# Kernel tuning notes

Hardware: AMD Instinct MI355X
Metric: run time of the kernel (lower is better)

## Reference

```python
import jax, jax.numpy as jnp
import numpy as np

R = 2        # pixel-shuffle upscale
CN = 32      # channel_nums
COL = 3      # colors
NM = 6       # module_nums (2 convs each -> 12 backbone convs)
QMAX_A = 255.0   # uint8 activation fake-quant range
QMAX_W = 127.0   # int8 (narrow) weight fake-quant range


def fq_act(x, s):
    # Brevitas Uint8ActPerTensorFloat fake-quant with STE
    v = x / s
    q = jnp.clip(jnp.round(v), 0.0, QMAX_A)
    return s * (v + jax.lax.stop_gradient(q - v))


def fq_w(w, s):
    # Int8WeightPerTensorFloat (symmetric, narrow range) fake-quant with STE
    v = w / s
    q = jnp.clip(jnp.round(v), -QMAX_W, QMAX_W)
    return s * (v + jax.lax.stop_gradient(q - v))


def conv3(x, w, b):
    y = jax.lax.conv_general_dilated(
        x, w, window_strides=(1, 1), padding=((1, 1), (1, 1)),
        dimension_numbers=("NCHW", "OIHW", "NCHW"))
    return y + b[None, :, None, None]


def qblock(x, w, b, sw, act_s):
    # QuantConv3X3: quant_in -> quant conv (+bias) -> QuantReLU (relu + quant)
    xq = fq_act(x, act_s)
    y = conv3(xq, fq_w(w, sw), b)
    y = jax.nn.relu(y)
    return fq_act(y, act_s)


def pixel_shuffle(x, r):
    B, C, H, W = x.shape
    c = C // (r * r)
    x = x.reshape(B, c, r, r, H, W)
    x = x.transpose(0, 1, 4, 2, 5, 3)   # B, c, H, r, W, r
    return x.reshape(B, c, H * r, W * r)


def _forward(x, head_w, head_b, head_sw, bb_w, bb_b, bb_sw, tr_w, tr_b, tr_sw, act_s):
    y0 = qblock(x, head_w, head_b, head_sw, act_s)

    def step(y, p):
        w, b, sw = p
        return qblock(y, w, b, sw, act_s), None

    y, _ = jax.lax.scan(step, y0, (bb_w, bb_b, bb_sw))
    y = qblock(y + y0, tr_w, tr_b, tr_sw, act_s)   # act_type='linear' still hits QuantReLU branch
    y = jnp.clip(y, 0.0, 255.0)
    return pixel_shuffle(y, R)


def setup_inputs() -> dict:
    key = jax.random.key(0)
    ks = jax.random.split(key, 4)
    B, H, W = 8, 256, 256
    x = jax.random.uniform(ks[0], (B, COL, H, W), dtype=jnp.float32) * 255.0
    head_w = jax.random.normal(ks[1], (CN, COL, 3, 3), dtype=jnp.float32) * 0.05
    head_b = jnp.zeros((CN,), jnp.float32)
    bb_w = jax.random.normal(ks[2], (2 * NM, CN, CN, 3, 3), dtype=jnp.float32) * 0.05
    bb_b = jnp.zeros((2 * NM, CN), jnp.float32)
    tr_w = jax.random.normal(ks[3], (COL * R * R, CN, 3, 3), dtype=jnp.float32) * 0.05
    tr_b = jnp.zeros((COL * R * R,), jnp.float32)
    head_sw = jnp.max(jnp.abs(head_w)) / QMAX_W
    bb_sw = jnp.max(jnp.abs(bb_w), axis=(1, 2, 3, 4)) / QMAX_W
    tr_sw = jnp.max(jnp.abs(tr_w)) / QMAX_W
    act_s = jnp.float32(1.0)
    return dict(x=x, head_w=head_w, head_b=head_b, head_sw=head_sw,
                bb_w=bb_w, bb_b=bb_b, bb_sw=bb_sw,
                tr_w=tr_w, tr_b=tr_b, tr_sw=tr_sw, act_s=act_s)


def reference(x, head_w, head_b, head_sw, bb_w, bb_b, bb_sw, tr_w, tr_b, tr_sw, act_s):
    return _forward(x, head_w, head_b, head_sw, bb_w, bb_b, bb_sw, tr_w, tr_b, tr_sw, act_s)
```

## Files before the change

### kernel.cpp

```cpp
#include <hip/hip_runtime.h>

typedef __bf16 bf16x8 __attribute__((ext_vector_type(8)));
typedef float  f32x16 __attribute__((ext_vector_type(16)));

__global__ __launch_bounds__(256) void quantw_kernel(
    const float* __restrict__ src, float* __restrict__ dst,
    const float* __restrict__ sw, int per_layer_sw, int OC, int ICK, int total)
{
    int i = blockIdx.x * 256 + threadIdx.x;
    if (i >= total) return;
    int per = OC * ICK;
    int l = i / per;
    int rem = i - l * per;
    int oc = rem / ICK;
    int k = rem - oc * ICK;
    float s = sw[per_layer_sw ? l : 0];
    float v = rintf(src[i] / s);
    v = fminf(fmaxf(v, -127.0f), 127.0f);
    dst[l * per + k * OC + oc] = v;
}

__global__ __launch_bounds__(256) void packb_kernel(
    const float* __restrict__ src, unsigned short* __restrict__ dst,
    const float* __restrict__ sw, int per_layer_sw, int OC_real, int total)
{
    int i = blockIdx.x * 256 + threadIdx.x;
    if (i >= total) return;
    int l   = i / 9216;
    int r   = i - l * 9216;
    int s   = r >> 9;
    int lane = (r >> 3) & 63;
    int j   = r & 7;
    int k   = s * 16 + ((lane >> 5) << 3) + j;
    int tap = k >> 5;
    int ic  = k & 31;
    int oc  = lane & 31;
    unsigned short v = 0;
    if (oc < OC_real) {
        float scale = sw[per_layer_sw ? l : 0];
        float w = src[((l * OC_real + oc) * 32 + ic) * 9 + tap];
        float q = rintf(w / scale);
        q = fminf(fmaxf(q, -127.0f), 127.0f);
        union { float f; unsigned int u; } cv; cv.f = q;
        v = (unsigned short)(cv.u >> 16);
    }
    dst[i] = v;
}

__global__ __launch_bounds__(256) void head_kernel(
    const float* __restrict__ x, const float* __restrict__ wq,
    const float* __restrict__ bias, const float* __restrict__ sw_ptr,
    const float* __restrict__ s_ptr, unsigned char* __restrict__ out)
{
    __shared__ unsigned char tile[3][10][34];
    const int tid = threadIdx.x;
    const int x0 = blockIdx.x * 32;
    const int y0 = blockIdx.y * 8;
    const int b  = blockIdx.z;
    const float s = s_ptr[0];

    for (int ch = 0; ch < 3; ++ch) {
        const int base = (b * 3 + ch) << 16;
        for (int p = tid; p < 10 * 34; p += 256) {
            int r = p / 34, c = p - r * 34;
            int gy = y0 + r - 1, gx = x0 + c - 1;
            unsigned char v = 0;
            if ((unsigned)gy < 256u && (unsigned)gx < 256u) {
                float xv = x[base + (gy << 8) + gx];
                float q = (s == 1.0f) ? xv : (xv / s);
                q = rintf(q);
                q = fminf(fmaxf(q, 0.0f), 255.0f);
                v = (unsigned char)q;
            }
            tile[ch][r][c] = v;
        }
    }
    __syncthreads();

    const int c = tid & 31, r = tid >> 5;
    float acc[32];
    #pragma unroll
    for (int i = 0; i < 32; ++i) acc[i] = 0.0f;

    #pragma unroll
    for (int ic = 0; ic < 3; ++ic) {
        float a[9];
        #pragma unroll
        for (int dy = 0; dy < 3; ++dy)
            #pragma unroll
            for (int dx = 0; dx < 3; ++dx)
                a[dy * 3 + dx] = (float)tile[ic][r + dy][c + dx];
        #pragma unroll
        for (int t = 0; t < 9; ++t) {
            const float* wrow = wq + (ic * 9 + t) * 32;
            #pragma unroll
            for (int oc = 0; oc < 32; ++oc)
                acc[oc] = fmaf(a[t], wrow[oc], acc[oc]);
        }
    }

    const float alpha = s * sw_ptr[0];
    unsigned int w8[8] = {0,0,0,0,0,0,0,0};
    #pragma unroll
    for (int oc = 0; oc < 32; ++oc) {
        float y = fmaf(alpha, acc[oc], bias[oc]);
        y = fmaxf(y, 0.0f);
        float v = (s == 1.0f) ? y : (y / s);
        v = rintf(v);
        v = fminf(fmaxf(v, 0.0f), 255.0f);
        w8[oc >> 2] |= ((unsigned int)(unsigned char)v) << (8 * (oc & 3));
    }
    uint4* dst = (uint4*)(out + (size_t)((((b << 8) + (y0 + r)) << 8) + (x0 + c)) * 32);
    dst[0] = make_uint4(w8[0], w8[1], w8[2], w8[3]);
    dst[1] = make_uint4(w8[4], w8[5], w8[6], w8[7]);
}

template<bool FINAL>
__global__ __launch_bounds__(256, 4) void qconv_mfma_kernel(
    const unsigned char* __restrict__ in,
    const unsigned char* __restrict__ resid,
    const unsigned short* __restrict__ Bp,
    const float* __restrict__ bias,
    const float* __restrict__ sw_ptr, int sw_idx,
    const float* __restrict__ s_ptr,
    void* __restrict__ out)
{
    __shared__ uint4 aT[2448];
    const int tid = threadIdx.x;
    const int x0 = blockIdx.x << 5;
    const int y0 = blockIdx.y << 4;
    const int b  = blockIdx.z;

    #pragma unroll
    for (int it = 0; it < 5; ++it) {
        int ci = tid + it * 256;
        if (ci < 1224) {
            int yt  = ci / 68;
            int rem = ci - yt * 68;
            int xt  = rem >> 1;
            int ch  = rem & 1;
            int gy = y0 + yt - 1;
            int gx = x0 + xt - 1;
            uint4 raw = make_uint4(0, 0, 0, 0);
            uint4 res = make_uint4(0, 0, 0, 0);
            if ((unsigned)gy < 256u && (unsigned)gx < 256u) {
                size_t off = (size_t)((((b << 8) + gy) << 8) + gx) * 32 + (ch << 4);
                raw = *(const uint4*)(in + off);
                if (FINAL) res = *(const uint4*)(resid + off);
            }
            unsigned int ow[8];
            const unsigned int* rw = (const unsigned int*)&raw;
            const unsigned int* rr = (const unsigned int*)&res;
            #pragma unroll
            for (int w = 0; w < 4; ++w) {
                unsigned int v = rw[w], rv = rr[w];
                #pragma unroll
                for (int hb = 0; hb < 2; ++hb) {
                    unsigned int a0 = (v >> (16 * hb)) & 0xffu;
                    unsigned int a1 = (v >> (16 * hb + 8)) & 0xffu;
                    if (FINAL) {
                        a0 += (rv >> (16 * hb)) & 0xffu;      if (a0 > 255u) a0 = 255u;
                        a1 += (rv >> (16 * hb + 8)) & 0xffu;  if (a1 > 255u) a1 = 255u;
                    }
                    union { float f; unsigned int u; } c0, c1;
                    c0.f = (float)a0; c1.f = (float)a1;
                    ow[2 * w + hb] = (c0.u >> 16) | (c1.u & 0xffff0000u);
                }
            }
            int swz  = (xt & 3) ^ ((xt >> 2) & 3);
            int base = (yt * 34 + xt) << 2;
            aT[base + (((ch << 1) + 0) ^ swz)] = make_uint4(ow[0], ow[1], ow[2], ow[3]);
            aT[base + (((ch << 1) + 1) ^ swz)] = make_uint4(ow[4], ow[5], ow[6], ow[7]);
        }
    }
    __syncthreads();

    const int lane = tid & 63;
    const int wid  = tid >> 6;
    const int px   = lane & 31;
    const int half = lane >> 5;
    const int py0  = wid << 2;

    const bf16x8* Wg = (const bf16x8*)Bp;

    f32x16 acc[4];
    #pragma unroll
    for (int p = 0; p < 4; ++p)
        #pragma unroll
        for (int i = 0; i < 16; ++i) acc[p][i] = 0.0f;

    #pragma unroll
    for (int ich = 0; ich < 2; ++ich) {
        const int cb = (ich << 1) + half;
        #pragma unroll
        for (int dx = 0; dx < 3; ++dx) {
            const int xt = px + dx;
            const int cbs = cb ^ ((xt & 3) ^ ((xt >> 2) & 3));
            bf16x8 af[6];
            #pragma unroll
            for (int yl = 0; yl < 6; ++yl)
                af[yl] = *(const bf16x8*)&aT[((py0 + yl) * 34 + xt) * 4 + cbs];
            #pragma unroll
            for (int dy = 0; dy < 3; ++dy) {
                bf16x8 wfr = Wg[(((dy * 3 + dx) << 1) + ich) * 64 + lane];
                acc[0] = __builtin_amdgcn_mfma_f32_32x32x16_bf16(wfr, af[dy + 0], acc[0], 0, 0, 0);
                acc[1] = __builtin_amdgcn_mfma_f32_32x32x16_bf16(wfr, af[dy + 1], acc[1], 0, 0, 0);
                acc[2] = __builtin_amdgcn_mfma_f32_32x32x16_bf16(wfr, af[dy + 2], acc[2], 0, 0, 0);
                acc[3] = __builtin_amdgcn_mfma_f32_32x32x16_bf16(wfr, af[dy + 3], acc[3], 0, 0, 0);
            }
        }
    }

    const float s = s_ptr[0];
    const float alpha = s * sw_ptr[sw_idx];
    const int gx = x0 + px;

    if (!FINAL) {
        float bv[16];
        #pragma unroll
        for (int r = 0; r < 16; ++r)
            bv[r] = bias[(r & 3) + ((r >> 2) << 3) + (half << 2)];
        #pragma unroll
        for (int py = 0; py < 4; ++py) {
            const int gy = y0 + py0 + py;
            unsigned char* pout = (unsigned char*)out + (((size_t)((((b << 8) + gy) << 8) + gx)) << 5);
            #pragma unroll
            for (int q = 0; q < 4; ++q) {
                unsigned int wv = 0;
                #pragma unroll
                for (int j = 0; j < 4; ++j) {
                    float y = fmaf(alpha, acc[py][4 * q + j], bv[4 * q + j]);
                    y = fmaxf(y, 0.0f);
                    float v = (s == 1.0f) ? y : (y / s);
                    v = rintf(v);
                    v = fminf(fmaxf(v, 0.0f), 255.0f);
                    wv |= ((unsigned int)v) << (8 * j);
                }
                *(unsigned int*)(pout + 8 * q + 4 * half) = wv;
            }
        }
    } else {
        #pragma unroll
        for (int py = 0; py < 4; ++py) {
            const int gy = y0 + py0 + py;
            #pragma unroll
            for (int r = 0; r < 16; ++r) {
                const int oc = (r & 3) + ((r >> 2) << 3) + (half << 2);
                if (oc < 12) {
                    float y = fmaf(alpha, acc[py][r], bias[oc]);
                    y = fmaxf(y, 0.0f);
                    float v = (s == 1.0f) ? y : (y / s);
                    v = rintf(v);
                    v = fminf(fmaxf(v, 0.0f), 255.0f);
                    float o = (s == 1.0f) ? v : fminf(fmaxf(s * v, 0.0f), 255.0f);
                    const int cc = oc >> 2, r1 = (oc >> 1) & 1, r2 = oc & 1;
                    ((float*)out)[(size_t)(((b * 3 + cc) << 9) + (gy << 1) + r1) * 512 + (gx << 1) + r2] = o;
                }
            }
        }
    }
}

extern "C" void kernel_launch(void* const* d_in, const int* in_sizes, int n_in,
                              void* d_out, int out_size, void* d_ws, size_t ws_size,
                              hipStream_t stream) {
    const float* x       = (const float*)d_in[0];
    const float* head_w  = (const float*)d_in[1];
    const float* head_b  = (const float*)d_in[2];
    const float* head_sw = (const float*)d_in[3];
    const float* bb_w    = (const float*)d_in[4];
    const float* bb_b    = (const float*)d_in[5];
    const float* bb_sw   = (const float*)d_in[6];
    const float* tr_w    = (const float*)d_in[7];
    const float* tr_b    = (const float*)d_in[8];
    const float* tr_sw   = (const float*)d_in[9];
    const float* act_s   = (const float*)d_in[10];

    char* ws = (char*)d_ws;
    unsigned char* buf0 = (unsigned char*)ws;
    unsigned char* buf1 = buf0 + 16777216;
    unsigned char* buf2 = buf1 + 16777216;
    float* wqH = (float*)(ws + 50331648);
    unsigned short* BpB = (unsigned short*)(ws + 50331648 + 4096);
    unsigned short* BpT = BpB + 110592;

    quantw_kernel<<<(864 + 255) / 256, 256, 0, stream>>>(head_w, wqH, head_sw, 0, 32, 27, 864);
    packb_kernel<<<(110592 + 255) / 256, 256, 0, stream>>>(bb_w, BpB, bb_sw, 1, 32, 110592);
    packb_kernel<<<(9216 + 255) / 256, 256, 0, stream>>>(tr_w, BpT, tr_sw, 0, 12, 9216);

    head_kernel<<<dim3(8, 32, 8), 256, 0, stream>>>(x, wqH, head_b, head_sw, act_s, buf0);

    dim3 gridB(8, 16, 8);
    const unsigned char* cur = buf0;
    unsigned char* nxt = buf1;
    for (int l = 0; l < 12; ++l) {
        qconv_mfma_kernel<false><<<gridB, 256, 0, stream>>>(
            cur, nullptr, BpB + l * 9216, bb_b + l * 32, bb_sw, l, act_s, (void*)nxt);
        cur = nxt;
        nxt = (nxt == buf1) ? buf2 : buf1;
    }

    qconv_mfma_kernel<true><<<gridB, 256, 0, stream>>>(
        cur, buf0, BpT, tr_b, tr_sw, 0, act_s, d_out);
}
```

Before: 349.5 us.

## Switch conv MFMA from bf16 to int8 with offset-encoded activations

Activations are stored as uint8 XOR 0x80, which reinterprets them as signed int8 values offset by -128. The convolutions now use i32 32x32x32 int8 MFMA instead of bf16 MFMA, halving the shared tile size and the MFMA count per K. The -128 offset is corrected exactly through a precomputed per-output-channel sum of the quantized weights folded into the bias. The aim is to remove the bf16 conversion in tile loading and double the MFMA throughput, at the cost of an extra small weight-sum kernel and different swizzle and layout code.

```diff
diff --git a/kernel.cpp b/kernel.cpp
--- a/kernel.cpp
+++ b/kernel.cpp
@@ -1,7 +1,7 @@
 #include <hip/hip_runtime.h>
 
-typedef __bf16 bf16x8 __attribute__((ext_vector_type(8)));
-typedef float  f32x16 __attribute__((ext_vector_type(16)));
+typedef int i32x4  __attribute__((ext_vector_type(4)));
+typedef int i32x16 __attribute__((ext_vector_type(16)));
 
 __global__ __launch_bounds__(256) void quantw_kernel(
     const float* __restrict__ src, float* __restrict__ dst,
@@ -20,31 +20,53 @@
     dst[l * per + k * OC + oc] = v;
 }
 
-__global__ __launch_bounds__(256) void packb_kernel(
-    const float* __restrict__ src, unsigned short* __restrict__ dst,
+__global__ __launch_bounds__(256) void packw_i8_kernel(
+    const float* __restrict__ src, signed char* __restrict__ dst,
     const float* __restrict__ sw, int per_layer_sw, int OC_real, int total)
 {
     int i = blockIdx.x * 256 + threadIdx.x;
     if (i >= total) return;
     int l   = i / 9216;
     int r   = i - l * 9216;
-    int s   = r >> 9;
-    int lane = (r >> 3) & 63;
-    int j   = r & 7;
-    int k   = s * 16 + ((lane >> 5) << 3) + j;
-    int tap = k >> 5;
-    int ic  = k & 31;
+    int tap = r >> 10;
+    int r2  = r & 1023;
+    int lane = r2 >> 4;
+    int j   = r2 & 15;
     int oc  = lane & 31;
-    unsigned short v = 0;
+    int ic  = ((lane >> 5) << 4) + j;
+    signed char v = 0;
     if (oc < OC_real) {
-        float scale = sw[per_layer_sw ? l : 0];
-        float w = src[((l * OC_real + oc) * 32 + ic) * 9 + tap];
-        float q = rintf(w / scale);
+        float s = sw[per_layer_sw ? l : 0];
+        float q = rintf(src[((l * OC_real + oc) * 32 + ic) * 9 + tap] / s);
         q = fminf(fmaxf(q, -127.0f), 127.0f);
-        union { float f; unsigned int u; } cv; cv.f = q;
-        v = (unsigned short)(cv.u >> 16);
+        v = (signed char)(int)q;
     }
     dst[i] = v;
+}
+
+__global__ __launch_bounds__(256) void wsum_kernel(
+    const float* __restrict__ bb_w, const float* __restrict__ bb_sw,
+    const float* __restrict__ tr_w, const float* __restrict__ tr_sw,
+    float* __restrict__ wsum)
+{
+    int t = blockIdx.x * 256 + threadIdx.x;
+    if (t >= 416) return;
+    int l = t >> 5, oc = t & 31;
+    float sum = 0.0f;
+    if (l < 12) {
+        float s = bb_sw[l];
+        for (int k = 0; k < 288; ++k) {
+            float q = rintf(bb_w[(l * 32 + oc) * 288 + k] / s);
+            sum += fminf(fmaxf(q, -127.0f), 127.0f);
+        }
+    } else if (oc < 12) {
+        float s = tr_sw[0];
+        for (int k = 0; k < 288; ++k) {
+            float q = rintf(tr_w[oc * 288 + k] / s);
+            sum += fminf(fmaxf(q, -127.0f), 127.0f);
+        }
+    }
+    wsum[t] = sum;
 }
 
 __global__ __launch_bounds__(256) void head_kernel(
@@ -111,21 +133,22 @@
         w8[oc >> 2] |= ((unsigned int)(unsigned char)v) << (8 * (oc & 3));
     }
     uint4* dst = (uint4*)(out + (size_t)((((b << 8) + (y0 + r)) << 8) + (x0 + c)) * 32);
-    dst[0] = make_uint4(w8[0], w8[1], w8[2], w8[3]);
-    dst[1] = make_uint4(w8[4], w8[5], w8[6], w8[7]);
+    dst[0] = make_uint4(w8[0] ^ 0x80808080u, w8[1] ^ 0x80808080u, w8[2] ^ 0x80808080u, w8[3] ^ 0x80808080u);
+    dst[1] = make_uint4(w8[4] ^ 0x80808080u, w8[5] ^ 0x80808080u, w8[6] ^ 0x80808080u, w8[7] ^ 0x80808080u);
 }
 
 template<bool FINAL>
-__global__ __launch_bounds__(256, 4) void qconv_mfma_kernel(
+__global__ __launch_bounds__(256, 4) void qconv_i8_kernel(
     const unsigned char* __restrict__ in,
     const unsigned char* __restrict__ resid,
-    const unsigned short* __restrict__ Bp,
+    const signed char* __restrict__ Wp,
     const float* __restrict__ bias,
+    const float* __restrict__ wsum,
     const float* __restrict__ sw_ptr, int sw_idx,
     const float* __restrict__ s_ptr,
     void* __restrict__ out)
 {
-    __shared__ uint4 aT[2448];
+    __shared__ unsigned char aT[19584];
     const int tid = threadIdx.x;
     const int x0 = blockIdx.x << 5;
     const int y0 = blockIdx.y << 4;
@@ -135,42 +158,35 @@
     for (int it = 0; it < 5; ++it) {
         int ci = tid + it * 256;
         if (ci < 1224) {
-            int yt  = ci / 68;
-            int rem = ci - yt * 68;
-            int xt  = rem >> 1;
-            int ch  = rem & 1;
-            int gy = y0 + yt - 1;
-            int gx = x0 + xt - 1;
-            uint4 raw = make_uint4(0, 0, 0, 0);
-            uint4 res = make_uint4(0, 0, 0, 0);
+            int row = (ci * 241) >> 14;
+            int rem = ci - row * 68;
+            int xt = rem >> 1, hf = rem & 1;
+            int gy = y0 + row - 1, gx = x0 + xt - 1;
+            uint4 v = make_uint4(0x80808080u, 0x80808080u, 0x80808080u, 0x80808080u);
             if ((unsigned)gy < 256u && (unsigned)gx < 256u) {
-                size_t off = (size_t)((((b << 8) + gy) << 8) + gx) * 32 + (ch << 4);
-                raw = *(const uint4*)(in + off);
-                if (FINAL) res = *(const uint4*)(resid + off);
-            }
-            unsigned int ow[8];
-            const unsigned int* rw = (const unsigned int*)&raw;
-            const unsigned int* rr = (const unsigned int*)&res;
-            #pragma unroll
-            for (int w = 0; w < 4; ++w) {
-                unsigned int v = rw[w], rv = rr[w];
-                #pragma unroll
-                for (int hb = 0; hb < 2; ++hb) {
-                    unsigned int a0 = (v >> (16 * hb)) & 0xffu;
-                    unsigned int a1 = (v >> (16 * hb + 8)) & 0xffu;
-                    if (FINAL) {
-                        a0 += (rv >> (16 * hb)) & 0xffu;      if (a0 > 255u) a0 = 255u;
-                        a1 += (rv >> (16 * hb + 8)) & 0xffu;  if (a1 > 255u) a1 = 255u;
+                size_t off = (size_t)((((b << 8) + gy) << 8) + gx) * 32 + (hf << 4);
+                v = *(const uint4*)(in + off);
+                if (FINAL) {
+                    uint4 rv = *(const uint4*)(resid + off);
+                    unsigned int* vp = (unsigned int*)&v;
+                    const unsigned int* rp = (const unsigned int*)&rv;
+                    #pragma unroll
+                    for (int w = 0; w < 4; ++w) {
+                        unsigned int xw = vp[w], yw = rp[w], ow = 0;
+                        #pragma unroll
+                        for (int bb = 0; bb < 4; ++bb) {
+                            int xs = (int)(signed char)(xw >> (8 * bb));
+                            int ys = (int)(signed char)(yw >> (8 * bb));
+                            int t = xs + ys + 128;
+                            if (t > 127) t = 127;
+                            ow |= ((unsigned int)(t & 255)) << (8 * bb);
+                        }
+                        vp[w] = ow;
                     }
-                    union { float f; unsigned int u; } c0, c1;
-                    c0.f = (float)a0; c1.f = (float)a1;
-                    ow[2 * w + hb] = (c0.u >> 16) | (c1.u & 0xffff0000u);
                 }
             }
-            int swz  = (xt & 3) ^ ((xt >> 2) & 3);
-            int base = (yt * 34 + xt) << 2;
-            aT[base + (((ch << 1) + 0) ^ swz)] = make_uint4(ow[0], ow[1], ow[2], ow[3]);
-            aT[base + (((ch << 1) + 1) ^ swz)] = make_uint4(ow[4], ow[5], ow[6], ow[7]);
+            int cs = rem ^ ((rem >> 3) & 7);
+            *(uint4*)&aT[(row * 68 + cs) << 4] = v;
         }
     }
     __syncthreads();
@@ -178,48 +194,44 @@
     const int lane = tid & 63;
     const int wid  = tid >> 6;
     const int px   = lane & 31;
-    const int half = lane >> 5;
+    const int khf  = lane >> 5;
     const int py0  = wid << 2;
-
-    const bf16x8* Wg = (const bf16x8*)Bp;
-
-    f32x16 acc[4];
+    const int gx   = x0 + px;
+
+    i32x16 acc[4];
     #pragma unroll
     for (int p = 0; p < 4; ++p)
         #pragma unroll
-        for (int i = 0; i < 16; ++i) acc[p][i] = 0.0f;
-
-    #pragma unroll
-    for (int ich = 0; ich < 2; ++ich) {
-        const int cb = (ich << 1) + half;
-        #pragma unroll
-        for (int dx = 0; dx < 3; ++dx) {
-            const int xt = px + dx;
-            const int cbs = cb ^ ((xt & 3) ^ ((xt >> 2) & 3));
-            bf16x8 af[6];
-            #pragma unroll
-            for (int yl = 0; yl < 6; ++yl)
-                af[yl] = *(const bf16x8*)&aT[((py0 + yl) * 34 + xt) * 4 + cbs];
-            #pragma unroll
-            for (int dy = 0; dy < 3; ++dy) {
-                bf16x8 wfr = Wg[(((dy * 3 + dx) << 1) + ich) * 64 + lane];
-                acc[0] = __builtin_amdgcn_mfma_f32_32x32x16_bf16(wfr, af[dy + 0], acc[0], 0, 0, 0);
-                acc[1] = __builtin_amdgcn_mfma_f32_32x32x16_bf16(wfr, af[dy + 1], acc[1], 0, 0, 0);
-                acc[2] = __builtin_amdgcn_mfma_f32_32x32x16_bf16(wfr, af[dy + 2], acc[2], 0, 0, 0);
-                acc[3] = __builtin_amdgcn_mfma_f32_32x32x16_bf16(wfr, af[dy + 3], acc[3], 0, 0, 0);
-            }
+        for (int i = 0; i < 16; ++i) acc[p][i] = 0;
+
+    #pragma unroll
+    for (int dx = 0; dx < 3; ++dx) {
+        const int c  = ((px + dx) << 1) + khf;
+        const int cs = c ^ ((c >> 3) & 7);
+        i32x4 af[6];
+        #pragma unroll
+        for (int yl = 0; yl < 6; ++yl)
+            af[yl] = *(const i32x4*)&aT[((py0 + yl) * 68 + cs) << 4];
+        #pragma unroll
+        for (int dy = 0; dy < 3; ++dy) {
+            i32x4 wf = *(const i32x4*)(Wp + ((((dy * 3 + dx) << 6) + lane) << 4));
+            acc[0] = __builtin_amdgcn_mfma_i32_32x32x32_i8(wf, af[dy + 0], acc[0], 0, 0, 0);
+            acc[1] = __builtin_amdgcn_mfma_i32_32x32x32_i8(wf, af[dy + 1], acc[1], 0, 0, 0);
+            acc[2] = __builtin_amdgcn_mfma_i32_32x32x32_i8(wf, af[dy + 2], acc[2], 0, 0, 0);
+            acc[3] = __builtin_amdgcn_mfma_i32_32x32x32_i8(wf, af[dy + 3], acc[3], 0, 0, 0);
         }
     }
 
     const float s = s_ptr[0];
     const float alpha = s * sw_ptr[sw_idx];
-    const int gx = x0 + px;
 
     if (!FINAL) {
         float bv[16];
         #pragma unroll
-        for (int r = 0; r < 16; ++r)
-            bv[r] = bias[(r & 3) + ((r >> 2) << 3) + (half << 2)];
+        for (int r = 0; r < 16; ++r) {
+            const int oc = (r & 3) + ((r >> 2) << 3) + (khf << 2);
+            bv[r] = fmaf(alpha * 128.0f, wsum[oc], bias[oc]);
+        }
         #pragma unroll
         for (int py = 0; py < 4; ++py) {
             const int gy = y0 + py0 + py;
@@ -229,14 +241,14 @@
                 unsigned int wv = 0;
                 #pragma unroll
                 for (int j = 0; j < 4; ++j) {
-                    float y = fmaf(alpha, acc[py][4 * q + j], bv[4 * q + j]);
+                    float y = fmaf(alpha, (float)acc[py][4 * q + j], bv[4 * q + j]);
                     y = fmaxf(y, 0.0f);
                     float v = (s == 1.0f) ? y : (y / s);
                     v = rintf(v);
                     v = fminf(fmaxf(v, 0.0f), 255.0f);
                     wv |= ((unsigned int)v) << (8 * j);
                 }
-                *(unsigned int*)(pout + 8 * q + 4 * half) = wv;
+                *(unsigned int*)(pout + 8 * q + 4 * khf) = wv ^ 0x80808080u;
             }
         }
     } else {
@@ -245,9 +257,10 @@
             const int gy = y0 + py0 + py;
             #pragma unroll
             for (int r = 0; r < 16; ++r) {
-                const int oc = (r & 3) + ((r >> 2) << 3) + (half << 2);
+                const int oc = (r & 3) + ((r >> 2) << 3) + (khf << 2);
                 if (oc < 12) {
-                    float y = fmaf(alpha, acc[py][r], bias[oc]);
+                    float y = fmaf(alpha, (float)acc[py][r],
+                                   fmaf(alpha * 128.0f, wsum[oc], bias[oc]));
                     y = fmaxf(y, 0.0f);
                     float v = (s == 1.0f) ? y : (y / s);
                     v = rintf(v);
@@ -281,12 +294,14 @@
     unsigned char* buf1 = buf0 + 16777216;
     unsigned char* buf2 = buf1 + 16777216;
     float* wqH = (float*)(ws + 50331648);
-    unsigned short* BpB = (unsigned short*)(ws + 50331648 + 4096);
-    unsigned short* BpT = BpB + 110592;
+    signed char* WpB = (signed char*)(ws + 50331648 + 4096);
+    signed char* WpT = WpB + 110592;
+    float* wsum = (float*)(ws + 50331648 + 4096 + 110592 + 9216);
 
     quantw_kernel<<<(864 + 255) / 256, 256, 0, stream>>>(head_w, wqH, head_sw, 0, 32, 27, 864);
-    packb_kernel<<<(110592 + 255) / 256, 256, 0, stream>>>(bb_w, BpB, bb_sw, 1, 32, 110592);
-    packb_kernel<<<(9216 + 255) / 256, 256, 0, stream>>>(tr_w, BpT, tr_sw, 0, 12, 9216);
+    packw_i8_kernel<<<(110592 + 255) / 256, 256, 0, stream>>>(bb_w, WpB, bb_sw, 1, 32, 110592);
+    packw_i8_kernel<<<(9216 + 255) / 256, 256, 0, stream>>>(tr_w, WpT, tr_sw, 0, 12, 9216);
+    wsum_kernel<<<2, 256, 0, stream>>>(bb_w, bb_sw, tr_w, tr_sw, wsum);
 
     head_kernel<<<dim3(8, 32, 8), 256, 0, stream>>>(x, wqH, head_b, head_sw, act_s, buf0);
 
@@ -294,12 +309,12 @@
     const unsigned char* cur = buf0;
     unsigned char* nxt = buf1;
     for (int l = 0; l < 12; ++l) {
-        qconv_mfma_kernel<false><<<gridB, 256, 0, stream>>>(
-            cur, nullptr, BpB + l * 9216, bb_b + l * 32, bb_sw, l, act_s, (void*)nxt);
+        qconv_i8_kernel<false><<<gridB, 256, 0, stream>>>(
+            cur, nullptr, WpB + l * 9216, bb_b + l * 32, wsum + l * 32, bb_sw, l, act_s, (void*)nxt);
         cur = nxt;
         nxt = (nxt == buf1) ? buf2 : buf1;
     }
 
-    qconv_mfma_kernel<true><<<gridB, 256, 0, stream>>>(
-        cur, buf0, BpT, tr_b, tr_sw, 0, act_s, d_out);
-}
+    qconv_i8_kernel<true><<<gridB, 256, 0, stream>>>(
+        cur, buf0, WpT, tr_b, wsum + 384, tr_sw, 0, act_s, d_out);
+}
```

Result: no change. 355.9 us (+1.9%).
